# Kernel optimization log

Hardware: AMD Instinct MI355X
Metric: run time of the kernel (lower is better)

The kernel has to match this reference:

```python
import jax, jax.numpy as jnp
import numpy as np


def setup_inputs() -> dict:
    key = jax.random.key(0)
    ks = jax.random.split(key, 8)
    B, C, H, W = 8, 512, 64, 64
    Co = C // 8
    s = 0.02  # weight init scale
    return {
        'x': jax.random.normal(ks[0], (B, C, H, W), jnp.float32),
        'Wq': jax.random.normal(ks[1], (Co, C), jnp.float32) * s,
        'bq': jnp.zeros((Co,), jnp.float32),
        'Wk': jax.random.normal(ks[2], (Co, C), jnp.float32) * s,
        'bk': jnp.zeros((Co,), jnp.float32),
        'Wv': jax.random.normal(ks[3], (C, C), jnp.float32) * s,
        'bv': jnp.zeros((C,), jnp.float32),
        'gamma': jax.random.normal(ks[4], (1,), jnp.float32) * 0.1,
    }


def reference(x, Wq, bq, Wk, bk, Wv, bv, gamma):
    B, C, H, W = x.shape
    # 1x1 convs == channel contractions
    q = jnp.einsum('oc,bchw->bohw', Wq, x) + bq[None, :, None, None]
    k = jnp.einsum('oc,bchw->bohw', Wk, x) + bk[None, :, None, None]
    v = jnp.einsum('oc,bchw->bohw', Wv, x) + bv[None, :, None, None]
    # column (H-axis) energies, diagonal masked to -inf to avoid double count
    eH = jnp.einsum('bohw,boiw->bhwi', q, k)  # [B,H,W,H2]
    diag_mask = jnp.where(jnp.eye(H, dtype=bool), -jnp.inf, 0.0)  # [H,H2]
    eH = eH + diag_mask[None, :, None, :]
    # row (W-axis) energies
    eW = jnp.einsum('bohw,bohj->bhwj', q, k)  # [B,H,W,W2]
    # joint softmax over concatenated H+W axis
    attn = jax.nn.softmax(jnp.concatenate([eH, eW], axis=-1), axis=-1)
    aH, aW = attn[..., :H], attn[..., H:]
    out = jnp.einsum('bciw,bhwi->bchw', v, aH) + jnp.einsum('bchj,bhwj->bchw', v, aW)
    return gamma[0] * out + x
```

## Files before the change

kernel.cpp:

```cpp
#include <hip/hip_runtime.h>
#include <hip/hip_bf16.h>

#define NB 8
#define NC 512
#define NO 64
#define NH 64
#define NW 64
#define NHW 4096

typedef __attribute__((ext_vector_type(8))) short bf16x8;
typedef __attribute__((ext_vector_type(4))) float f32x4;

__device__ __forceinline__ void gload16(const void* g, void* l) {
    __builtin_amdgcn_global_load_lds(
        (const __attribute__((address_space(1))) void*)g,
        (__attribute__((address_space(3))) void*)l, 16, 0, 0);
}

__device__ __forceinline__ short f2bf_bits(float f) {
    __hip_bfloat16 h = __float2bfloat16(f);
    short s; __builtin_memcpy(&s, &h, 2); return s;
}
__device__ __forceinline__ float bfbits_to_f(short s) {
    unsigned int u = ((unsigned int)(unsigned short)s) << 16;
    float f; __builtin_memcpy(&f, &u, 4); return f;
}

__global__ __launch_bounds__(256) void pack_w(
    const float* __restrict__ Wq, const float* __restrict__ bq,
    const float* __restrict__ Wk, const float* __restrict__ bk,
    const float* __restrict__ Wv, const float* __restrict__ bv,
    __hip_bfloat16* __restrict__ Wbf, float* __restrict__ bias_all)
{
    const int row = blockIdx.x;
    const int t = threadIdx.x;
    const float* src; float bias;
    if (row < 64)       { src = Wq + row*NC;        bias = bq[row]; }
    else if (row < 128) { src = Wk + (row-64)*NC;   bias = bk[row-64]; }
    else                { src = Wv + (row-128)*NC;  bias = bv[row-128]; }
    for (int i = t; i < NC; i += 256)
        Wbf[(size_t)row*NC + i] = __float2bfloat16(src[i]);
    if (t == 0) bias_all[row] = bias;
}

__global__ __launch_bounds__(256) void qkv_fused(
    const float* __restrict__ x, const __hip_bfloat16* __restrict__ Wbf,
    const float* __restrict__ bias_all,
    __hip_bfloat16* __restrict__ qkT2, __hip_bfloat16* __restrict__ vb)
{
    __shared__ __align__(16) char Bs[2][16384];
    const int t = threadIdx.x;
    const int lane = t & 63;
    const int wv = t >> 6;
    const int wm = wv >> 1, wn = wv & 1;
    const int fr = lane & 15, fg = lane >> 4;
    const int hw0 = blockIdx.x * 128;
    const int y   = blockIdx.y;
    const int b   = blockIdx.z;
    const int o0s = (y == 4) ? 0 : (128 + y*128);
    const float* xb = x + (size_t)b*NC*NHW + hw0;
    const int oct = t >> 5, hwg = t & 31;
    const __hip_bfloat16* Wrow = Wbf + (size_t)o0s*NC;

    float4 xrA[8], xrB[8];

#define LOADB(j, XR) do {                                                   \
        const float* gp = xb + (size_t)((j)*64 + oct*8)*NHW + hwg*4;        \
        _Pragma("unroll")                                                   \
        for (int e = 0; e < 8; ++e)                                         \
            XR[e] = *(const float4*)(gp + (size_t)e*NHW);                   \
    } while (0)
#define WRITEB(XR, buf) do {                                                \
        _Pragma("unroll")                                                   \
        for (int d = 0; d < 4; ++d) {                                       \
            int row = hwg*4 + d;                                            \
            bf16x8 wv8;                                                     \
            _Pragma("unroll")                                               \
            for (int e = 0; e < 8; ++e)                                     \
                wv8[e] = f2bf_bits(((const float*)&XR[e])[d]);              \
            int slot = oct ^ (row & 7) ^ ((row >> 3) & 7);                  \
            *(bf16x8*)(Bs[buf] + row*128 + (slot << 4)) = wv8;              \
        }                                                                   \
    } while (0)
#define BSLOT(c, gl) (((gl) ^ ((c) & 7) ^ (((c) >> 3) & 7)) << 4)

    LOADB(0, xrA);
    LOADB(1, xrB);
    WRITEB(xrA, 0);
    __syncthreads();

    f32x4 acc[4][4] = {};

    #pragma unroll
    for (int ks = 0; ks < 8; ++ks) {
        const int cur = ks & 1;
        if (ks < 6) {
            if ((ks & 1) == 0) { LOADB(ks+2, xrA); } else { LOADB(ks+2, xrB); }
        }
        #pragma unroll
        for (int kk = 0; kk < 2; ++kk) {
            const int gl = kk*4 + fg;
            bf16x8 m1[4], n1[4];
            if (y == 4) {
                #pragma unroll
                for (int mf = 0; mf < 4; ++mf) {
                    int r = wm*64 + mf*16 + fr;
                    m1[mf] = *(const bf16x8*)(Bs[cur] + r*128 + BSLOT(r, gl));
                }
                #pragma unroll
                for (int nf = 0; nf < 4; ++nf) {
                    int c = wn*64 + nf*16 + fr;
                    n1[nf] = *(const bf16x8*)(Wrow + (size_t)c*NC + ks*64 + gl*8);
                }
            } else {
                #pragma unroll
                for (int mf = 0; mf < 4; ++mf) {
                    int r = wm*64 + mf*16 + fr;
                    m1[mf] = *(const bf16x8*)(Wrow + (size_t)r*NC + ks*64 + gl*8);
                }
                #pragma unroll
                for (int nf = 0; nf < 4; ++nf) {
                    int c = wn*64 + nf*16 + fr;
                    n1[nf] = *(const bf16x8*)(Bs[cur] + c*128 + BSLOT(c, gl));
                }
            }
            #pragma unroll
            for (int mf = 0; mf < 4; ++mf)
                #pragma unroll
                for (int nf = 0; nf < 4; ++nf)
                    acc[mf][nf] = __builtin_amdgcn_mfma_f32_16x16x32_bf16(
                        m1[mf], n1[nf], acc[mf][nf], 0, 0, 0);
        }
        if (ks < 7) {
            if (ks & 1) { WRITEB(xrA, (ks+1)&1); } else { WRITEB(xrB, (ks+1)&1); }
            __syncthreads();
        }
    }
#undef LOADB
#undef WRITEB
#undef BSLOT

    if (y < 4) {
        #pragma unroll
        for (int mf = 0; mf < 4; ++mf) {
            #pragma unroll
            for (int reg = 0; reg < 4; ++reg) {
                int o = o0s + wm*64 + mf*16 + (lane >> 4)*4 + reg;
                float bias = bias_all[o];
                size_t rowbase = ((size_t)b*NC + (o - 128))*NHW;
                #pragma unroll
                for (int nf = 0; nf < 4; ++nf) {
                    int hw = hw0 + wn*64 + nf*16 + (lane & 15);
                    vb[rowbase + hw] = __float2bfloat16(acc[mf][nf][reg] + bias);
                }
            }
        }
    } else {
        #pragma unroll
        for (int mf = 0; mf < 4; ++mf) {
            #pragma unroll
            for (int reg = 0; reg < 4; ++reg) {
                int hwl = wm*64 + mf*16 + (lane >> 4)*4 + reg;
                size_t rbase = ((size_t)b*NHW + hw0 + hwl)*128;
                #pragma unroll
                for (int nf = 0; nf < 4; ++nf) {
                    int col = wn*64 + nf*16 + (lane & 15);
                    qkT2[rbase + col] = __float2bfloat16(acc[mf][nf][reg] + bias_all[col]);
                }
            }
        }
    }
}

__global__ __launch_bounds__(256) void transpose_hw(
    const __hip_bfloat16* __restrict__ src_, __hip_bfloat16* __restrict__ dst_,
    int nch)
{
    __shared__ __align__(16) short tile[4][64*64];
    const int t = threadIdx.x, wv = t >> 6, lane = t & 63;
    const int c = blockIdx.x*4 + wv, b = blockIdx.y;
    const __hip_bfloat16* src = src_ + ((size_t)(b*nch + c))*NHW;
    __hip_bfloat16* dst = dst_ + ((size_t)(b*nch + c))*NHW;
    short* tl = tile[wv];
    #pragma unroll
    for (int s = 0; s < 8; ++s) {
        int i = s*8 + (lane>>3), w0 = (lane&7)*8;
        bf16x8 vv = *(const bf16x8*)(src + i*64 + w0);
        *(bf16x8*)&tl[i*64 + (((w0>>3) ^ ((i>>3)&7)) << 3)] = vv;
    }
    __syncthreads();
    #pragma unroll
    for (int s = 0; s < 8; ++s) {
        int w = s*8 + (lane>>3), i0 = (lane&7)*8;
        bf16x8 ov;
        #pragma unroll
        for (int d = 0; d < 8; ++d)
            ov[d] = tl[(i0+d)*64 + (((w>>3) ^ (lane&7)) << 3) + (w&7)];
        *(bf16x8*)(dst + w*64 + i0) = ov;
    }
}

__global__ __launch_bounds__(256) void scores_mfma(
    const __hip_bfloat16* __restrict__ qkT2,
    __hip_bfloat16* __restrict__ rawH, __hip_bfloat16* __restrict__ rawW)
{
    __shared__ __align__(16) char Qs[64*128];
    __shared__ __align__(16) char Ks[64*128];
    const int t = threadIdx.x, lane = t & 63, wv = t >> 6;
    const int wm = wv >> 1, wn = wv & 1;
    const int fr = lane & 15, fg = lane >> 4;
    const int s = blockIdx.x, y = blockIdx.y, b = blockIdx.z;
    const __hip_bfloat16* base = qkT2 + (size_t)b * NHW * 128;
    #pragma unroll
    for (int i = 0; i < 2; ++i) {
        int linear = i*256 + t;
        int r = linear >> 3, g = linear & 7;
        int gk = (g ^ (r & 7)) * 8;
        size_t ro = (y == 0) ? ((size_t)(r*64 + s) * 128)
                             : ((size_t)(s*64 + r) * 128);
        gload16(base + ro + gk,      Qs + linear*16);
        gload16(base + ro + 64 + gk, Ks + linear*16);
    }
    __syncthreads();
    f32x4 acc[2][2] = {};
    #pragma unroll
    for (int kk = 0; kk < 2; ++kk) {
        const int gl = kk*4 + fg;
        bf16x8 qf[2], kf[2];
        #pragma unroll
        for (int mf = 0; mf < 2; ++mf) {
            int r = wm*32 + mf*16 + fr;
            qf[mf] = *(const bf16x8*)(Qs + r*128 + ((gl ^ (r & 7)) << 4));
        }
        #pragma unroll
        for (int nf = 0; nf < 2; ++nf) {
            int c = wn*32 + nf*16 + fr;
            kf[nf] = *(const bf16x8*)(Ks + c*128 + ((gl ^ (c & 7)) << 4));
        }
        #pragma unroll
        for (int mf = 0; mf < 2; ++mf)
            #pragma unroll
            for (int nf = 0; nf < 2; ++nf)
                acc[mf][nf] = __builtin_amdgcn_mfma_f32_16x16x32_bf16(
                    qf[mf], kf[nf], acc[mf][nf], 0, 0, 0);
    }
    __hip_bfloat16* dst = (y == 0) ? rawH : rawW;
    const size_t dbase = ((size_t)(b*64 + s)) * 4096;
    #pragma unroll
    for (int mf = 0; mf < 2; ++mf) {
        #pragma unroll
        for (int reg = 0; reg < 4; ++reg) {
            int row = wm*32 + mf*16 + (lane >> 4)*4 + reg;
            #pragma unroll
            for (int nf = 0; nf < 2; ++nf) {
                int col = wn*32 + nf*16 + (lane & 15);
                dst[dbase + (size_t)row*64 + col] = __float2bfloat16(acc[mf][nf][reg]);
            }
        }
    }
}

__global__ __launch_bounds__(256) void softmax_ab(
    const __hip_bfloat16* __restrict__ rawH, const __hip_bfloat16* __restrict__ rawW,
    __hip_bfloat16* __restrict__ aHb, __hip_bfloat16* __restrict__ aWb)
{
    __shared__ float sH[64][65];
    __shared__ float sW[64][65];
    __shared__ float red[8][64];
    const int t = threadIdx.x;
    const int w = t & 63, p = t >> 6;
    const int hb = blockIdx.x, b = blockIdx.y;
    #pragma unroll
    for (int i2 = 0; i2 < 2; ++i2) {
        int linear = i2*256 + t;
        int ww = linear >> 3, g = linear & 7;
        bf16x8 hv = *(const bf16x8*)(rawH + (((size_t)(b*64 + ww))*64 + hb)*64 + g*8);
        bf16x8 wvv = *(const bf16x8*)(rawW + (((size_t)(b*64 + hb))*64 + ww)*64 + g*8);
        #pragma unroll
        for (int e = 0; e < 8; ++e) {
            sH[ww][g*8+e] = bfbits_to_f(hv[e]);
            sW[ww][g*8+e] = bfbits_to_f(wvv[e]);
        }
    }
    __syncthreads();
    if (t < 64) sH[t][hb] = -1e30f;
    __syncthreads();
    float m = -1e30f;
    #pragma unroll
    for (int z = 0; z < 32; ++z) {
        float val = (p < 2) ? sH[w][p*32+z] : sW[w][(p-2)*32+z];
        m = fmaxf(m, val);
    }
    red[p][w] = m;
    __syncthreads();
    float M = fmaxf(fmaxf(red[0][w], red[1][w]), fmaxf(red[2][w], red[3][w]));
    float ssum = 0.f;
    #pragma unroll
    for (int z = 0; z < 32; ++z) {
        float* slot = (p < 2) ? &sH[w][p*32+z] : &sW[w][(p-2)*32+z];
        float e = __expf(*slot - M);
        ssum += e;
        *slot = e;
    }
    red[4+p][w] = ssum;
    __syncthreads();
    float S = red[4][w] + red[5][w] + red[6][w] + red[7][w];
    float rinv = 1.f / S;
    if (p < 2) {
        size_t base = (((size_t)b*NH + w)*NH + hb)*NO + p*32;
        #pragma unroll
        for (int zz = 0; zz < 4; ++zz) {
            bf16x8 pk;
            #pragma unroll
            for (int d = 0; d < 8; ++d)
                pk[d] = f2bf_bits(sH[w][p*32 + zz*8 + d] * rinv);
            *(bf16x8*)(aHb + base + zz*8) = pk;
        }
    } else {
        size_t base = (((size_t)b*NH + hb)*NH + w)*NO + (p-2)*32;
        #pragma unroll
        for (int zz = 0; zz < 4; ++zz) {
            bf16x8 pk;
            #pragma unroll
            for (int d = 0; d < 8; ++d)
                pk[d] = f2bf_bits(sW[w][(p-2)*32 + zz*8 + d] * rinv);
            *(bf16x8*)(aWb + base + zz*8) = pk;
        }
    }
}

__global__ __launch_bounds__(256) void col_mfma(
    const __hip_bfloat16* __restrict__ vT, const __hip_bfloat16* __restrict__ aH,
    __hip_bfloat16* __restrict__ PT)
{
    __shared__ __align__(16) char As[64*128];
    __shared__ __align__(16) char Bs[256*128];
    const int t = threadIdx.x, lane = t & 63, wn = t >> 6;
    const int fr = lane & 15, fg = lane >> 4;
    const int w = blockIdx.x, chalf = blockIdx.y, b = blockIdx.z;
    const __hip_bfloat16* Ag = aH + ((size_t)(b*NH + w))*4096;
    const __hip_bfloat16* Bg = vT + ((size_t)(b*NC + chalf*256))*NHW + w*64;
    #pragma unroll
    for (int s = 0; s < 2; ++s) {
        int linear = s*256 + t;
        int r = linear >> 3, g = linear & 7;
        gload16(Ag + r*64 + ((g ^ (r&7)) * 8), As + linear*16);
    }
    #pragma unroll
    for (int s = 0; s < 8; ++s) {
        int linear = s*256 + t;
        int r = linear >> 3, g = linear & 7;
        gload16(Bg + (size_t)r*NHW + ((g ^ (r&7)) * 8), Bs + linear*16);
    }
    __syncthreads();
    f32x4 acc[4][4] = {};
    #pragma unroll
    for (int kk = 0; kk < 2; ++kk) {
        int gl = kk*4 + fg;
        bf16x8 af[4], bfv[4];
        #pragma unroll
        for (int mf = 0; mf < 4; ++mf) {
            int r = mf*16 + fr;
            af[mf] = *(const bf16x8*)(As + r*128 + ((gl ^ (r&7)) << 4));
        }
        #pragma unroll
        for (int nf = 0; nf < 4; ++nf) {
            int c = wn*64 + nf*16 + fr;
            bfv[nf] = *(const bf16x8*)(Bs + c*128 + ((gl ^ (c&7)) << 4));
        }
        #pragma unroll
        for (int mf = 0; mf < 4; ++mf)
            #pragma unroll
            for (int nf = 0; nf < 4; ++nf)
                acc[mf][nf] = __builtin_amdgcn_mfma_f32_16x16x32_bf16(
                    af[mf], bfv[nf], acc[mf][nf], 0, 0, 0);
    }
    const size_t base = ((size_t)(b*NH + w))*64*512 + chalf*256;
    #pragma unroll
    for (int mf = 0; mf < 4; ++mf) {
        #pragma unroll
        for (int reg = 0; reg < 4; ++reg) {
            int hh = mf*16 + (lane >> 4)*4 + reg;
            #pragma unroll
            for (int nf = 0; nf < 4; ++nf) {
                int cc = wn*64 + nf*16 + (lane & 15);
                PT[base + (size_t)hh*512 + cc] = __float2bfloat16(acc[mf][nf][reg]);
            }
        }
    }
}

__global__ __launch_bounds__(256) void row_mfma(
    const __hip_bfloat16* __restrict__ vb, const __hip_bfloat16* __restrict__ aW,
    const __hip_bfloat16* __restrict__ PT, const float* __restrict__ x,
    const float* __restrict__ gamma, float* __restrict__ out)
{
    __shared__ __align__(16) char Ws[64*128];
    __shared__ __align__(16) char Vs[128*128];
    __shared__ __align__(16) short PTs[64*136];
    const int t = threadIdx.x, lane = t & 63, wm = t >> 6;
    const int fr = lane & 15, fg = lane >> 4;
    const int h = blockIdx.x, cq = blockIdx.y, b = blockIdx.z;
    const int c0 = cq*128;
    const __hip_bfloat16* Ag = aW + ((size_t)(b*NH + h))*4096;
    const __hip_bfloat16* Vg = vb + ((size_t)(b*NC + c0))*NHW + h*64;
    #pragma unroll
    for (int s = 0; s < 2; ++s) {
        int linear = s*256 + t;
        int r = linear >> 3, g = linear & 7;
        gload16(Ag + r*64 + ((g ^ (r&7)) * 8), Ws + linear*16);
    }
    #pragma unroll
    for (int s = 0; s < 4; ++s) {
        int linear = s*256 + t;
        int r = linear >> 3, g = linear & 7;
        gload16(Vg + (size_t)r*NHW + ((g ^ (r&7)) * 8), Vs + linear*16);
    }
    #pragma unroll
    for (int s = 0; s < 4; ++s) {
        int idx = s*256 + t;
        int ww = idx >> 4, cg = idx & 15;
        bf16x8 pv = *(const bf16x8*)(PT + (((size_t)(b*NH + ww))*64 + h)*512 + c0 + cg*8);
        *(bf16x8*)&PTs[ww*136 + cg*8] = pv;
    }
    __syncthreads();
    f32x4 acc[2][4] = {};
    #pragma unroll
    for (int kk = 0; kk < 2; ++kk) {
        int gl = kk*4 + fg;
        bf16x8 vf[2], wf[4];
        #pragma unroll
        for (int mf = 0; mf < 2; ++mf) {
            int c = wm*32 + mf*16 + fr;
            vf[mf] = *(const bf16x8*)(Vs + c*128 + ((gl ^ (c&7)) << 4));
        }
        #pragma unroll
        for (int nf = 0; nf < 4; ++nf) {
            int ww = nf*16 + fr;
            wf[nf] = *(const bf16x8*)(Ws + ww*128 + ((gl ^ (ww&7)) << 4));
        }
        #pragma unroll
        for (int mf = 0; mf < 2; ++mf)
            #pragma unroll
            for (int nf = 0; nf < 4; ++nf)
                acc[mf][nf] = __builtin_amdgcn_mfma_f32_16x16x32_bf16(
                    vf[mf], wf[nf], acc[mf][nf], 0, 0, 0);
    }
    const float g = gamma[0];
    #pragma unroll
    for (int mf = 0; mf < 2; ++mf) {
        #pragma unroll
        for (int reg = 0; reg < 4; ++reg) {
            int cl = wm*32 + mf*16 + (lane >> 4)*4 + reg;
            size_t rowbase = ((size_t)(b*NC + c0 + cl)*NH + h)*NW;
            #pragma unroll
            for (int nf = 0; nf < 4; ++nf) {
                int ww = nf*16 + (lane & 15);
                float ptv = bfbits_to_f(PTs[ww*136 + cl]);
                out[rowbase + ww] = g*(acc[mf][nf][reg] + ptv) + x[rowbase + ww];
            }
        }
    }
}

extern "C" void kernel_launch(void* const* d_in, const int* in_sizes, int n_in,
                              void* d_out, int out_size, void* d_ws, size_t ws_size,
                              hipStream_t stream) {
    (void)in_sizes; (void)n_in; (void)out_size; (void)ws_size;
    const float* x     = (const float*)d_in[0];
    const float* Wq    = (const float*)d_in[1];
    const float* bq    = (const float*)d_in[2];
    const float* Wk    = (const float*)d_in[3];
    const float* bk    = (const float*)d_in[4];
    const float* Wv    = (const float*)d_in[5];
    const float* bv    = (const float*)d_in[6];
    const float* gamma = (const float*)d_in[7];
    float* out = (float*)d_out;

    char* p = (char*)d_ws;
    __hip_bfloat16* Wbf  = (__hip_bfloat16*)(p);
    float* bias_all      = (float*)(p + 655360);
    __hip_bfloat16* qkT2 = (__hip_bfloat16*)(p + 657920);
    __hip_bfloat16* vb   = (__hip_bfloat16*)(p + 9046528);
    __hip_bfloat16* vT   = (__hip_bfloat16*)(p + 42600960);
    __hip_bfloat16* aHb  = (__hip_bfloat16*)(p + 76155392);
    __hip_bfloat16* aWb  = (__hip_bfloat16*)(p + 80349696);
    __hip_bfloat16* PT   = (__hip_bfloat16*)(p + 84544000);
    __hip_bfloat16* rawH = PT;
    __hip_bfloat16* rawW = (__hip_bfloat16*)(p + 84544000 + 8388608);

    pack_w<<<dim3(640), 256, 0, stream>>>(Wq, bq, Wk, bk, Wv, bv, Wbf, bias_all);
    qkv_fused<<<dim3(32, 5, NB), 256, 0, stream>>>(x, Wbf, bias_all, qkT2, vb);
    transpose_hw<<<dim3(128, NB), 256, 0, stream>>>(vb, vT, NC);
    scores_mfma<<<dim3(64, 2, NB), 256, 0, stream>>>(qkT2, rawH, rawW);
    softmax_ab<<<dim3(NH, NB), 256, 0, stream>>>(rawH, rawW, aHb, aWb);
    col_mfma<<<dim3(NW, 2, NB), 256, 0, stream>>>(vT, aHb, PT);
    row_mfma<<<dim3(NH, 4, NB), 256, 0, stream>>>(vb, aWb, PT, x, gamma, out);
}
```

Before: 137.3 us.

## Keep full x tile resident in LDS and loop over all output tiles per block

```diff
diff --git a/kernel.cpp b/kernel.cpp
--- a/kernel.cpp
+++ b/kernel.cpp
@@ -43,133 +43,150 @@
     if (t == 0) bias_all[row] = bias;
 }
 
-__global__ __launch_bounds__(256) void qkv_fused(
+__global__ __launch_bounds__(512) void qkv_mega2(
     const float* __restrict__ x, const __hip_bfloat16* __restrict__ Wbf,
     const float* __restrict__ bias_all,
     __hip_bfloat16* __restrict__ qkT2, __hip_bfloat16* __restrict__ vb)
 {
-    __shared__ __align__(16) char Bs[2][16384];
+    __shared__ __align__(16) char Bs[131072];
+    __shared__ __align__(16) char As[2][16384];
     const int t = threadIdx.x;
     const int lane = t & 63;
     const int wv = t >> 6;
-    const int wm = wv >> 1, wn = wv & 1;
+    const int wm = wv >> 2, wn = wv & 3;
     const int fr = lane & 15, fg = lane >> 4;
     const int hw0 = blockIdx.x * 128;
-    const int y   = blockIdx.y;
-    const int b   = blockIdx.z;
-    const int o0s = (y == 4) ? 0 : (128 + y*128);
+    const int b   = blockIdx.y;
     const float* xb = x + (size_t)b*NC*NHW + hw0;
-    const int oct = t >> 5, hwg = t & 31;
-    const __hip_bfloat16* Wrow = Wbf + (size_t)o0s*NC;
-
-    float4 xrA[8], xrB[8];
+    const int oct = t >> 6, hwp = t & 63;
+
+    typedef __attribute__((ext_vector_type(2))) float f32x2;
+    f32x2 xrA[8], xrB[8];
 
 #define LOADB(j, XR) do {                                                   \
-        const float* gp = xb + (size_t)((j)*64 + oct*8)*NHW + hwg*4;        \
+        const float* gp = xb + (size_t)((j)*64 + oct*8)*NHW + hwp*2;        \
         _Pragma("unroll")                                                   \
         for (int e = 0; e < 8; ++e)                                         \
-            XR[e] = *(const float4*)(gp + (size_t)e*NHW);                   \
+            XR[e] = *(const f32x2*)(gp + (size_t)e*NHW);                    \
     } while (0)
-#define WRITEB(XR, buf) do {                                                \
+#define WRITEB(j, XR) do {                                                  \
         _Pragma("unroll")                                                   \
-        for (int d = 0; d < 4; ++d) {                                       \
-            int row = hwg*4 + d;                                            \
+        for (int d = 0; d < 2; ++d) {                                       \
+            int row = hwp*2 + d;                                            \
             bf16x8 wv8;                                                     \
             _Pragma("unroll")                                               \
-            for (int e = 0; e < 8; ++e)                                     \
-                wv8[e] = f2bf_bits(((const float*)&XR[e])[d]);              \
-            int slot = oct ^ (row & 7) ^ ((row >> 3) & 7);                  \
-            *(bf16x8*)(Bs[buf] + row*128 + (slot << 4)) = wv8;              \
+            for (int e = 0; e < 8; ++e) wv8[e] = f2bf_bits(XR[e][d]);       \
+            int slot = (j)*8 + (oct ^ (row & 7) ^ ((row >> 3) & 7));        \
+            *(bf16x8*)(Bs + row*1024 + (slot << 4)) = wv8;                  \
         }                                                                   \
     } while (0)
-#define BSLOT(c, gl) (((gl) ^ ((c) & 7) ^ (((c) >> 3) & 7)) << 4)
-
-    LOADB(0, xrA);
-    LOADB(1, xrB);
-    WRITEB(xrA, 0);
-    __syncthreads();
-
-    f32x4 acc[4][4] = {};
-
-    #pragma unroll
-    for (int ks = 0; ks < 8; ++ks) {
-        const int cur = ks & 1;
-        if (ks < 6) {
-            if ((ks & 1) == 0) { LOADB(ks+2, xrA); } else { LOADB(ks+2, xrB); }
-        }
-        #pragma unroll
-        for (int kk = 0; kk < 2; ++kk) {
-            const int gl = kk*4 + fg;
-            bf16x8 m1[4], n1[4];
-            if (y == 4) {
-                #pragma unroll
-                for (int mf = 0; mf < 4; ++mf) {
-                    int r = wm*64 + mf*16 + fr;
-                    m1[mf] = *(const bf16x8*)(Bs[cur] + r*128 + BSLOT(r, gl));
+#define BSLOT(c, gl, ks) ((((ks)*8 + ((gl) ^ ((c) & 7) ^ (((c) >> 3) & 7))) << 4))
+#define STAGE_A(o0s, ksrc, buf) do {                                        \
+        _Pragma("unroll")                                                   \
+        for (int s = 0; s < 2; ++s) {                                       \
+            int linear = s*512 + t;                                         \
+            int row = linear >> 3, g = linear & 7;                          \
+            int gk = (g ^ (row & 7)) * 8;                                   \
+            gload16(Wbf + (size_t)((o0s) + row)*NC + (ksrc)*64 + gk,        \
+                    As[buf] + linear*16);                                   \
+        }                                                                   \
+    } while (0)
+
+    STAGE_A(128, 0, 0);
+    LOADB(0, xrA); LOADB(1, xrB);
+    WRITEB(0, xrA); LOADB(2, xrA);
+    WRITEB(1, xrB); LOADB(3, xrB);
+    WRITEB(2, xrA); LOADB(4, xrA);
+    WRITEB(3, xrB); LOADB(5, xrB);
+    WRITEB(4, xrA); LOADB(6, xrA);
+    WRITEB(5, xrB); LOADB(7, xrB);
+    WRITEB(6, xrA);
+    WRITEB(7, xrB);
+    __syncthreads();
+
+    int cur = 0;
+    for (int ot = 0; ot < 5; ++ot) {
+        const bool qk = (ot == 4);
+        const int o0s = qk ? 0 : (128 + ot*128);
+        f32x4 acc[4][2] = {};
+        for (int ks = 0; ks < 8; ++ks) {
+            const int nxt = cur ^ 1;
+            if (ks < 7)      STAGE_A(o0s, ks+1, nxt);
+            else if (ot < 4) STAGE_A((ot == 3) ? 0 : (128 + (ot+1)*128), 0, nxt);
+
+            #pragma unroll
+            for (int kk = 0; kk < 2; ++kk) {
+                const int gl = kk*4 + fg;
+                bf16x8 m1[4], n1[2];
+                if (!qk) {
+                    #pragma unroll
+                    for (int mf = 0; mf < 4; ++mf) {
+                        int r = wm*64 + mf*16 + fr;
+                        m1[mf] = *(const bf16x8*)(As[cur] + r*128 + ((gl ^ (r & 7)) << 4));
+                    }
+                    #pragma unroll
+                    for (int nf = 0; nf < 2; ++nf) {
+                        int c = wn*32 + nf*16 + fr;
+                        n1[nf] = *(const bf16x8*)(Bs + c*1024 + BSLOT(c, gl, ks));
+                    }
+                } else {
+                    #pragma unroll
+                    for (int mf = 0; mf < 4; ++mf) {
+                        int r = wm*64 + mf*16 + fr;
+                        m1[mf] = *(const bf16x8*)(Bs + r*1024 + BSLOT(r, gl, ks));
+                    }
+                    #pragma unroll
+                    for (int nf = 0; nf < 2; ++nf) {
+                        int c = wn*32 + nf*16 + fr;
+                        n1[nf] = *(const bf16x8*)(As[cur] + c*128 + ((gl ^ (c & 7)) << 4));
+                    }
                 }
                 #pragma unroll
-                for (int nf = 0; nf < 4; ++nf) {
-                    int c = wn*64 + nf*16 + fr;
-                    n1[nf] = *(const bf16x8*)(Wrow + (size_t)c*NC + ks*64 + gl*8);
-                }
-            } else {
+                for (int mf = 0; mf < 4; ++mf)
+                    #pragma unroll
+                    for (int nf = 0; nf < 2; ++nf)
+                        acc[mf][nf] = __builtin_amdgcn_mfma_f32_16x16x32_bf16(
+                            m1[mf], n1[nf], acc[mf][nf], 0, 0, 0);
+            }
+            __syncthreads();
+            cur ^= 1;
+        }
+
+        if (!qk) {
+            #pragma unroll
+            for (int mf = 0; mf < 4; ++mf) {
                 #pragma unroll
-                for (int mf = 0; mf < 4; ++mf) {
-                    int r = wm*64 + mf*16 + fr;
-                    m1[mf] = *(const bf16x8*)(Wrow + (size_t)r*NC + ks*64 + gl*8);
-                }
-                #pragma unroll
-                for (int nf = 0; nf < 4; ++nf) {
-                    int c = wn*64 + nf*16 + fr;
-                    n1[nf] = *(const bf16x8*)(Bs[cur] + c*128 + BSLOT(c, gl));
+                for (int reg = 0; reg < 4; ++reg) {
+                    int o = o0s + wm*64 + mf*16 + (lane >> 4)*4 + reg;
+                    float bias = bias_all[o];
+                    size_t rowbase = ((size_t)b*NC + (o - 128))*NHW;
+                    #pragma unroll
+                    for (int nf = 0; nf < 2; ++nf) {
+                        int hw = hw0 + wn*32 + nf*16 + (lane & 15);
+                        vb[rowbase + hw] = __float2bfloat16(acc[mf][nf][reg] + bias);
+                    }
                 }
             }
-            #pragma unroll
-            for (int mf = 0; mf < 4; ++mf)
+        } else {
+            #pragma unroll
+            for (int mf = 0; mf < 4; ++mf) {
                 #pragma unroll
-                for (int nf = 0; nf < 4; ++nf)
-                    acc[mf][nf] = __builtin_amdgcn_mfma_f32_16x16x32_bf16(
-                        m1[mf], n1[nf], acc[mf][nf], 0, 0, 0);
-        }
-        if (ks < 7) {
-            if (ks & 1) { WRITEB(xrA, (ks+1)&1); } else { WRITEB(xrB, (ks+1)&1); }
-            __syncthreads();
+                for (int reg = 0; reg < 4; ++reg) {
+                    int hwl = wm*64 + mf*16 + (lane >> 4)*4 + reg;
+                    size_t rbase = ((size_t)b*NHW + hw0 + hwl)*128;
+                    #pragma unroll
+                    for (int nf = 0; nf < 2; ++nf) {
+                        int col = wn*32 + nf*16 + (lane & 15);
+                        qkT2[rbase + col] = __float2bfloat16(acc[mf][nf][reg] + bias_all[col]);
+                    }
+                }
+            }
         }
     }
 #undef LOADB
 #undef WRITEB
 #undef BSLOT
-
-    if (y < 4) {
-        #pragma unroll
-        for (int mf = 0; mf < 4; ++mf) {
-            #pragma unroll
-            for (int reg = 0; reg < 4; ++reg) {
-                int o = o0s + wm*64 + mf*16 + (lane >> 4)*4 + reg;
-                float bias = bias_all[o];
-                size_t rowbase = ((size_t)b*NC + (o - 128))*NHW;
-                #pragma unroll
-                for (int nf = 0; nf < 4; ++nf) {
-                    int hw = hw0 + wn*64 + nf*16 + (lane & 15);
-                    vb[rowbase + hw] = __float2bfloat16(acc[mf][nf][reg] + bias);
-                }
-            }
-        }
-    } else {
-        #pragma unroll
-        for (int mf = 0; mf < 4; ++mf) {
-            #pragma unroll
-            for (int reg = 0; reg < 4; ++reg) {
-                int hwl = wm*64 + mf*16 + (lane >> 4)*4 + reg;
-                size_t rbase = ((size_t)b*NHW + hw0 + hwl)*128;
-                #pragma unroll
-                for (int nf = 0; nf < 4; ++nf) {
-                    int col = wn*64 + nf*16 + (lane & 15);
-                    qkT2[rbase + col] = __float2bfloat16(acc[mf][nf][reg] + bias_all[col]);
-                }
-            }
-        }
-    }
+#undef STAGE_A
 }
 
 __global__ __launch_bounds__(256) void transpose_hw(
@@ -490,7 +507,7 @@
     __hip_bfloat16* rawW = (__hip_bfloat16*)(p + 84544000 + 8388608);
 
     pack_w<<<dim3(640), 256, 0, stream>>>(Wq, bq, Wk, bk, Wv, bv, Wbf, bias_all);
-    qkv_fused<<<dim3(32, 5, NB), 256, 0, stream>>>(x, Wbf, bias_all, qkT2, vb);
+    qkv_mega2<<<dim3(32, NB), 512, 0, stream>>>(x, Wbf, bias_all, qkT2, vb);
     transpose_hw<<<dim3(128, NB), 256, 0, stream>>>(vb, vT, NC);
     scores_mfma<<<dim3(64, 2, NB), 256, 0, stream>>>(qkT2, rawH, rawW);
     softmax_ab<<<dim3(NH, NB), 256, 0, stream>>>(rawH, rawW, aHb, aWb);
```

Result: faster. 115.0 us (-16.3%).
